# Performance work log

Measured on AMD Instinct MI355X. Metric: run time of the kernel, lower is better.

The kernel has to match this reference:

```python
import jax, jax.numpy as jnp
import numpy as np

N_SRC, N_DST, E, D, OUT = 100000, 20000, 600000, 128, 128

def setup_inputs() -> dict:
    key = jax.random.key(0)
    k1, k2, k3, k4, k5 = jax.random.split(key, 5)
    h = jax.random.normal(k1, (N_SRC, D), dtype=jnp.float32)
    edge_src = jax.random.randint(k2, (E,), 0, N_SRC, dtype=jnp.int64)
    edge_dst = jax.random.randint(k3, (E,), 0, N_DST, dtype=jnp.int64)
    W = jax.random.normal(k4, (OUT, 2 * D), dtype=jnp.float32) * (1.0 / np.sqrt(2 * D))
    b = jax.random.normal(k5, (OUT,), dtype=jnp.float32) * 0.01
    return {"h": h, "edge_src": edge_src, "edge_dst": edge_dst, "W": W, "b": b, "n_dst": N_DST}

def reference(h, edge_src, edge_dst, W, b, n_dst):
    # dst nodes are the first n_dst src nodes (DGL block convention)
    h_dst = h[:n_dst]                                   # [n_dst, D]
    msgs = h[edge_src]                                  # gather: [E, D]
    agg = jax.ops.segment_sum(msgs, edge_dst, num_segments=n_dst)   # [n_dst, D]
    deg = jax.ops.segment_sum(jnp.ones(edge_src.shape, h.dtype), edge_dst, num_segments=n_dst)
    h_neigh = agg / jnp.maximum(deg, 1.0)[:, None]      # mean; 0-degree -> 0
    z = jnp.concatenate([h_dst, h_neigh], axis=1)       # [n_dst, 2D]
    return jax.nn.relu(z @ W.T + b)                     # [n_dst, OUT]
```

## Files before the change

kernel.cpp:

```cpp
#include <hip/hip_runtime.h>

#define DFEAT 128
#define KDIM  256
#define CAP   128
#define WSTR  264

typedef __attribute__((ext_vector_type(8))) short bf16x8;
typedef __attribute__((ext_vector_type(4))) float f32x4;

__device__ __forceinline__ float bflo(unsigned int u) {
    union { unsigned int i; float f; } v; v.i = u << 16; return v.f;
}
__device__ __forceinline__ float bfhi(unsigned int u) {
    union { unsigned int i; float f; } v; v.i = u & 0xffff0000u; return v.f;
}
__device__ __forceinline__ unsigned short f2bf(float f) {
    union { float f; unsigned int i; } v; v.f = f;
    unsigned int r = (v.i + 0x7fffu + ((v.i >> 16) & 1u)) >> 16;
    return (unsigned short)r;
}
__device__ __forceinline__ unsigned int pack2(float x, float y) {
    return ((unsigned int)f2bf(y) << 16) | (unsigned int)f2bf(x);
}
__device__ __forceinline__ uint4 cvt8(const float* p) {
    float4 a = *(const float4*)p;
    float4 b = *(const float4*)(p + 4);
    return make_uint4(pack2(a.x, a.y), pack2(a.z, a.w),
                      pack2(b.x, b.y), pack2(b.z, b.w));
}

__global__ __launch_bounds__(256) void prep_kernel(
    const float* __restrict__ h, const float* __restrict__ W,
    const int* __restrict__ esrc, const int* __restrict__ edst,
    unsigned short* __restrict__ hbf,
    unsigned short* __restrict__ z,
    unsigned short* __restrict__ Wbf,
    int* __restrict__ cnt, int* __restrict__ sorted,
    int E, int n_chunks, int B_C, int B_H)
{
    int blk = blockIdx.x;
    int tid = threadIdx.x;
    if (blk < B_C) {
        int e0 = blk * 1024 + tid;
        int d[4], s[4];
        bool ok[4];
        #pragma unroll
        for (int r = 0; r < 4; ++r) {
            int e = e0 + r * 256;
            ok[r] = (e < E);
            d[r] = ok[r] ? edst[e] : 0;
            s[r] = ok[r] ? esrc[e] : 0;
        }
        int pos[4];
        #pragma unroll
        for (int r = 0; r < 4; ++r)
            pos[r] = ok[r] ? atomicAdd(&cnt[d[r]], 1) : CAP;
        #pragma unroll
        for (int r = 0; r < 4; ++r)
            if (ok[r] && pos[r] < CAP)
                sorted[(size_t)d[r] * CAP + pos[r]] = s[r];
    } else if (blk < B_C + B_H) {
        int c0 = (blk - B_C) * 1024 + tid;
        #pragma unroll
        for (int r = 0; r < 4; ++r) {
            int t = c0 + r * 256;
            if (t < n_chunks) {
                uint4 v = cvt8(h + (size_t)t * 8);
                if (hbf) {
                    *(uint4*)(hbf + (size_t)t * 8) = v;
                } else {
                    int row = t >> 4;
                    int col = (t & 15) * 8;
                    *(uint4*)(z + (size_t)row * KDIM + col) = v;
                }
            }
        }
    } else {
        int t = (blk - B_C - B_H) * 256 + tid;
        *(uint4*)(Wbf + (size_t)t * 8) = cvt8(W + (size_t)t * 8);
    }
}

__global__ __launch_bounds__(256) void agg_bf16_kernel(
    const unsigned short* __restrict__ hbf, const int* __restrict__ cnt,
    const int* __restrict__ sorted, unsigned short* __restrict__ zn, int n_dst)
{
    int d = blockIdx.x * 4 + (threadIdx.x >> 6);
    if (d >= n_dst) return;
    int lane = threadIdx.x & 63;
    int c = cnt[d]; if (c > CAP) c = CAP;
    const int* seg = sorted + (size_t)d * CAP;
    float ax = 0.f, ay = 0.f;
    const unsigned int* hp = (const unsigned int*)hbf + lane;
    int i = 0;
    for (; i + 7 < c; i += 8) {
        int ix[8];
        #pragma unroll
        for (int r = 0; r < 8; ++r) ix[r] = seg[i + r];
        unsigned int u[8];
        #pragma unroll
        for (int r = 0; r < 8; ++r) u[r] = hp[(size_t)ix[r] * 64];
        #pragma unroll
        for (int r = 0; r < 8; ++r) { ax += bflo(u[r]); ay += bfhi(u[r]); }
    }
    for (; i + 3 < c; i += 4) {
        int i0 = seg[i],     i1 = seg[i + 1];
        int i2 = seg[i + 2], i3 = seg[i + 3];
        unsigned int u0 = hp[(size_t)i0 * 64], u1 = hp[(size_t)i1 * 64];
        unsigned int u2 = hp[(size_t)i2 * 64], u3 = hp[(size_t)i3 * 64];
        ax += bflo(u0) + bflo(u1) + bflo(u2) + bflo(u3);
        ay += bfhi(u0) + bfhi(u1) + bfhi(u2) + bfhi(u3);
    }
    for (; i < c; ++i) {
        unsigned int u = hp[(size_t)seg[i] * 64];
        ax += bflo(u); ay += bfhi(u);
    }
    float inv = 1.0f / fmaxf((float)c, 1.0f);
    ((unsigned int*)zn)[(size_t)d * 64 + lane] = pack2(ax * inv, ay * inv);
}

__global__ __launch_bounds__(256) void agg_f32_kernel(
    const float* __restrict__ h, const int* __restrict__ cnt,
    const int* __restrict__ sorted, unsigned short* __restrict__ z, int n_dst)
{
    int d = blockIdx.x * 4 + (threadIdx.x >> 6);
    if (d >= n_dst) return;
    int lane = threadIdx.x & 63;
    int c = cnt[d]; if (c > CAP) c = CAP;
    const int* seg = sorted + (size_t)d * CAP;
    float ax = 0.f, ay = 0.f;
    const float2* hp = (const float2*)h + lane;
    int i = 0;
    for (; i + 1 < c; i += 2) {
        int i0 = seg[i], i1 = seg[i + 1];
        float2 v0 = hp[(size_t)i0 * 64], v1 = hp[(size_t)i1 * 64];
        ax += v0.x + v1.x; ay += v0.y + v1.y;
    }
    for (; i < c; ++i) {
        float2 v = hp[(size_t)seg[i] * 64];
        ax += v.x; ay += v.y;
    }
    float inv = 1.0f / fmaxf((float)c, 1.0f);
    ((unsigned int*)z)[(size_t)d * 128 + 64 + lane] = pack2(ax * inv, ay * inv);
}

__global__ __launch_bounds__(256) void gemm_kernel(
    const unsigned short* __restrict__ alo, int slo,
    const unsigned short* __restrict__ ahi, int shi,
    const unsigned short* __restrict__ Wbf,
    const float* __restrict__ bias,
    float* __restrict__ out,
    int n_dst)
{
    __shared__ unsigned short Wl[DFEAT][WSTR];

    int tid  = threadIdx.x;
    int wave = tid >> 6;
    int lane = tid & 63;
    int quad = lane >> 4;
    int l16  = lane & 15;
    int m0   = blockIdx.x * 64 + wave * 16;

    #pragma unroll
    for (int i = 0; i < 16; ++i) {
        int u  = i * 256 + tid;
        int n  = u >> 5;
        int kq = (u & 31) * 8;
        *(uint4*)&Wl[n][kq] = *(const uint4*)(Wbf + (size_t)n * KDIM + kq);
    }

    int m_a = m0 + l16;
    if (m_a > n_dst - 1) m_a = n_dst - 1;

    f32x4 acc[8];
    #pragma unroll
    for (int ct = 0; ct < 8; ++ct) acc[ct] = (f32x4){0.f, 0.f, 0.f, 0.f};

    const unsigned short* plo = alo + (size_t)m_a * slo + quad * 8;
    const unsigned short* phi = ahi + (size_t)m_a * shi + quad * 8;

    __syncthreads();

    #pragma unroll
    for (int ks = 0; ks < 8; ++ks) {
        bf16x8 a = (ks < 4) ? *(const bf16x8*)(plo + ks * 32)
                            : *(const bf16x8*)(phi + (ks - 4) * 32);
        #pragma unroll
        for (int ct = 0; ct < 8; ++ct) {
            bf16x8 bb = *(const bf16x8*)&Wl[ct * 16 + l16][ks * 32 + quad * 8];
            acc[ct] = __builtin_amdgcn_mfma_f32_16x16x32_bf16(a, bb, acc[ct], 0, 0, 0);
        }
    }

    #pragma unroll
    for (int ct = 0; ct < 8; ++ct) {
        int n = ct * 16 + l16;
        float bc = bias[n];
        #pragma unroll
        for (int r = 0; r < 4; ++r) {
            int m = m0 + quad * 4 + r;
            if (m < n_dst)
                out[(size_t)m * DFEAT + n] = fmaxf(acc[ct][r] + bc, 0.0f);
        }
    }
}


extern "C" void kernel_launch(void* const* d_in, const int* in_sizes, int n_in,
                              void* d_out, int out_size, void* d_ws, size_t ws_size,
                              hipStream_t stream) {
    const float* h  = (const float*)d_in[0];
    const int* esrc = (const int*)d_in[1];
    const int* edst = (const int*)d_in[2];
    const float* W  = (const float*)d_in[3];
    const float* b  = (const float*)d_in[4];
    float* out      = (float*)d_out;

    const int E     = in_sizes[1];
    const int n_src = in_sizes[0] / DFEAT;
    const int n_dst = out_size / DFEAT;

    size_t hbf_bytes  = (size_t)n_src * DFEAT * 2;
    size_t zn_bytes   = (size_t)n_dst * DFEAT * 2;
    size_t wbf_bytes  = (size_t)DFEAT * KDIM * 2;
    size_t cnt_bytes  = (size_t)n_dst * sizeof(int);
    size_t srt_bytes  = (size_t)n_dst * CAP * sizeof(int);
    bool fast = ws_size >= hbf_bytes + zn_bytes + wbf_bytes + cnt_bytes + srt_bytes;

    char* p = (char*)d_ws;
    unsigned short *hbf, *zn, *Wbf;
    int *cnt, *sorted;
    if (fast) {
        hbf = (unsigned short*)p;            p += hbf_bytes;
        zn  = (unsigned short*)p;            p += zn_bytes;
        Wbf = (unsigned short*)p;            p += wbf_bytes;
        cnt = (int*)p;                       p += cnt_bytes;
        sorted = (int*)p;
    } else {
        hbf = nullptr; zn = nullptr;
        Wbf = (unsigned short*)p;            p += wbf_bytes;
        cnt = (int*)p;                       p += cnt_bytes;
        sorted = (int*)p;
    }

    unsigned short* z = (unsigned short*)d_out;

    (void)hipMemsetAsync(cnt, 0, cnt_bytes, stream);

    int n_chunks = (fast ? n_src : n_dst) * (DFEAT / 8);
    int B_C = (E + 1023) / 1024;
    int B_H = (n_chunks + 1023) / 1024;
    int B_W = (DFEAT * KDIM / 8) / 256;
    prep_kernel<<<B_C + B_H + B_W, 256, 0, stream>>>(
        h, W, esrc, edst, hbf, fast ? nullptr : z, Wbf, cnt, sorted,
        E, n_chunks, B_C, B_H);

    if (fast) {
        agg_bf16_kernel<<<(n_dst + 3) / 4, 256, 0, stream>>>(
            hbf, cnt, sorted, zn, n_dst);
        gemm_kernel<<<(n_dst + 63) / 64, 256, 0, stream>>>(
            hbf, DFEAT, zn, DFEAT, Wbf, b, out, n_dst);
    } else {
        agg_f32_kernel<<<(n_dst + 3) / 4, 256, 0, stream>>>(
            h, cnt, sorted, z, n_dst);
        gemm_kernel<<<(n_dst + 63) / 64, 256, 0, stream>>>(
            z, KDIM, z + DFEAT, KDIM, Wbf, b, out, n_dst);
    }
}
```

Before: 185.1 us.

## Fuse neighbor mean aggregation into GEMM via shared-memory tile

Merges the bf16 aggregation kernel and the GEMM kernel into one kernel. Each block aggregates 32 destination rows into LDS and then runs the MFMA GEMM on them directly, so the zn intermediate is never written to or read back from global memory and one launch is removed. In exchange, each block reloads the full 64KB W tile for only 32 rows, which doubles W staging traffic. Occupancy drops because of the larger LDS footprint, and each wave gathers 8 rows serially, which may reduce latency hiding for the gather.

New measurement: 208.1 us. 12.4% more time.

```diff
diff --git a/kernel.cpp b/kernel.cpp
--- a/kernel.cpp
+++ b/kernel.cpp
@@ -4,6 +4,8 @@
 #define KDIM  256
 #define CAP   128
 #define WSTR  264
+#define ZSTRU 68
+#define RTILE 32
 
 typedef __attribute__((ext_vector_type(8))) short bf16x8;
 typedef __attribute__((ext_vector_type(4))) float f32x4;
@@ -81,42 +83,105 @@
     }
 }
 
-__global__ __launch_bounds__(256) void agg_bf16_kernel(
-    const unsigned short* __restrict__ hbf, const int* __restrict__ cnt,
-    const int* __restrict__ sorted, unsigned short* __restrict__ zn, int n_dst)
+__global__ __launch_bounds__(256) void fused_kernel(
+    const unsigned short* __restrict__ hbf,
+    const int* __restrict__ cnt,
+    const int* __restrict__ sorted,
+    const unsigned short* __restrict__ Wbf,
+    const float* __restrict__ bias,
+    float* __restrict__ out,
+    int n_dst)
 {
-    int d = blockIdx.x * 4 + (threadIdx.x >> 6);
-    if (d >= n_dst) return;
-    int lane = threadIdx.x & 63;
-    int c = cnt[d]; if (c > CAP) c = CAP;
-    const int* seg = sorted + (size_t)d * CAP;
-    float ax = 0.f, ay = 0.f;
+    __shared__ unsigned short Wl[DFEAT][WSTR];
+    __shared__ unsigned int   znl[RTILE][ZSTRU];
+
+    const int tid  = threadIdx.x;
+    const int wave = tid >> 6;
+    const int lane = tid & 63;
+    const int quad = lane >> 4;
+    const int l16  = lane & 15;
+    const int m0   = blockIdx.x * RTILE;
+
+    #pragma unroll
+    for (int i = 0; i < 16; ++i) {
+        int u  = i * 256 + tid;
+        int n  = u >> 5;
+        int kq = (u & 31) * 8;
+        *(uint4*)&Wl[n][kq] = *(const uint4*)(Wbf + (size_t)n * KDIM + kq);
+    }
+
     const unsigned int* hp = (const unsigned int*)hbf + lane;
-    int i = 0;
-    for (; i + 7 < c; i += 8) {
-        int ix[8];
-        #pragma unroll
-        for (int r = 0; r < 8; ++r) ix[r] = seg[i + r];
-        unsigned int u[8];
-        #pragma unroll
-        for (int r = 0; r < 8; ++r) u[r] = hp[(size_t)ix[r] * 64];
-        #pragma unroll
-        for (int r = 0; r < 8; ++r) { ax += bflo(u[r]); ay += bfhi(u[r]); }
-    }
-    for (; i + 3 < c; i += 4) {
-        int i0 = seg[i],     i1 = seg[i + 1];
-        int i2 = seg[i + 2], i3 = seg[i + 3];
-        unsigned int u0 = hp[(size_t)i0 * 64], u1 = hp[(size_t)i1 * 64];
-        unsigned int u2 = hp[(size_t)i2 * 64], u3 = hp[(size_t)i3 * 64];
-        ax += bflo(u0) + bflo(u1) + bflo(u2) + bflo(u3);
-        ay += bfhi(u0) + bfhi(u1) + bfhi(u2) + bfhi(u3);
-    }
-    for (; i < c; ++i) {
-        unsigned int u = hp[(size_t)seg[i] * 64];
-        ax += bflo(u); ay += bfhi(u);
-    }
-    float inv = 1.0f / fmaxf((float)c, 1.0f);
-    ((unsigned int*)zn)[(size_t)d * 64 + lane] = pack2(ax * inv, ay * inv);
+    for (int t = 0; t < 8; ++t) {
+        int lr = wave * 8 + t;
+        int d  = m0 + lr;
+        if (d >= n_dst) break;
+        int c = cnt[d]; if (c > CAP) c = CAP;
+        const int* seg = sorted + (size_t)d * CAP;
+        float ax = 0.f, ay = 0.f;
+        int i = 0;
+        for (; i + 7 < c; i += 8) {
+            int ix[8];
+            #pragma unroll
+            for (int r = 0; r < 8; ++r) ix[r] = seg[i + r];
+            unsigned int u[8];
+            #pragma unroll
+            for (int r = 0; r < 8; ++r) u[r] = hp[(size_t)ix[r] * 64];
+            #pragma unroll
+            for (int r = 0; r < 8; ++r) { ax += bflo(u[r]); ay += bfhi(u[r]); }
+        }
+        for (; i + 3 < c; i += 4) {
+            int i0 = seg[i],     i1 = seg[i + 1];
+            int i2 = seg[i + 2], i3 = seg[i + 3];
+            unsigned int u0 = hp[(size_t)i0 * 64], u1 = hp[(size_t)i1 * 64];
+            unsigned int u2 = hp[(size_t)i2 * 64], u3 = hp[(size_t)i3 * 64];
+            ax += bflo(u0) + bflo(u1) + bflo(u2) + bflo(u3);
+            ay += bfhi(u0) + bfhi(u1) + bfhi(u2) + bfhi(u3);
+        }
+        for (; i < c; ++i) {
+            unsigned int u = hp[(size_t)seg[i] * 64];
+            ax += bflo(u); ay += bfhi(u);
+        }
+        float inv = 1.0f / fmaxf((float)c, 1.0f);
+        znl[lr][lane] = pack2(ax * inv, ay * inv);
+    }
+    __syncthreads();
+
+    const int r0 = (wave >> 1) * 16;
+    const int c0 = (wave & 1) * 64;
+    int m_a = m0 + r0 + l16;
+    if (m_a > n_dst - 1) m_a = n_dst - 1;
+
+    f32x4 acc[4];
+    #pragma unroll
+    for (int ct = 0; ct < 4; ++ct) acc[ct] = (f32x4){0.f, 0.f, 0.f, 0.f};
+
+    const unsigned short* plo = hbf + (size_t)m_a * DFEAT + quad * 8;
+    #pragma unroll
+    for (int ks = 0; ks < 8; ++ks) {
+        bf16x8 a;
+        if (ks < 4) {
+            a = *(const bf16x8*)(plo + ks * 32);
+        } else {
+            a = *(const bf16x8*)&znl[r0 + l16][(ks - 4) * 16 + quad * 4];
+        }
+        #pragma unroll
+        for (int ct = 0; ct < 4; ++ct) {
+            bf16x8 bb = *(const bf16x8*)&Wl[c0 + ct * 16 + l16][ks * 32 + quad * 8];
+            acc[ct] = __builtin_amdgcn_mfma_f32_16x16x32_bf16(a, bb, acc[ct], 0, 0, 0);
+        }
+    }
+
+    #pragma unroll
+    for (int ct = 0; ct < 4; ++ct) {
+        int n = c0 + ct * 16 + l16;
+        float bc = bias[n];
+        #pragma unroll
+        for (int r = 0; r < 4; ++r) {
+            int m = m0 + r0 + quad * 4 + r;
+            if (m < n_dst)
+                out[(size_t)m * DFEAT + n] = fmaxf(acc[ct][r] + bc, 0.0f);
+        }
+    }
 }
 
 __global__ __launch_bounds__(256) void agg_f32_kernel(
@@ -153,7 +218,6 @@
     int n_dst)
 {
     __shared__ unsigned short Wl[DFEAT][WSTR];
-
     int tid  = threadIdx.x;
     int wave = tid >> 6;
     int lane = tid & 63;
@@ -168,19 +232,14 @@
         int kq = (u & 31) * 8;
         *(uint4*)&Wl[n][kq] = *(const uint4*)(Wbf + (size_t)n * KDIM + kq);
     }
-
     int m_a = m0 + l16;
     if (m_a > n_dst - 1) m_a = n_dst - 1;
-
     f32x4 acc[8];
     #pragma unroll
     for (int ct = 0; ct < 8; ++ct) acc[ct] = (f32x4){0.f, 0.f, 0.f, 0.f};
-
     const unsigned short* plo = alo + (size_t)m_a * slo + quad * 8;
     const unsigned short* phi = ahi + (size_t)m_a * shi + quad * 8;
-
     __syncthreads();
-
     #pragma unroll
     for (int ks = 0; ks < 8; ++ks) {
         bf16x8 a = (ks < 4) ? *(const bf16x8*)(plo + ks * 32)
@@ -191,7 +250,6 @@
             acc[ct] = __builtin_amdgcn_mfma_f32_16x16x32_bf16(a, bb, acc[ct], 0, 0, 0);
         }
     }
-
     #pragma unroll
     for (int ct = 0; ct < 8; ++ct) {
         int n = ct * 16 + l16;
@@ -221,23 +279,21 @@
     const int n_dst = out_size / DFEAT;
 
     size_t hbf_bytes  = (size_t)n_src * DFEAT * 2;
-    size_t zn_bytes   = (size_t)n_dst * DFEAT * 2;
     size_t wbf_bytes  = (size_t)DFEAT * KDIM * 2;
     size_t cnt_bytes  = (size_t)n_dst * sizeof(int);
     size_t srt_bytes  = (size_t)n_dst * CAP * sizeof(int);
-    bool fast = ws_size >= hbf_bytes + zn_bytes + wbf_bytes + cnt_bytes + srt_bytes;
+    bool fast = ws_size >= hbf_bytes + wbf_bytes + cnt_bytes + srt_bytes;
 
     char* p = (char*)d_ws;
-    unsigned short *hbf, *zn, *Wbf;
+    unsigned short *hbf, *Wbf;
     int *cnt, *sorted;
     if (fast) {
         hbf = (unsigned short*)p;            p += hbf_bytes;
-        zn  = (unsigned short*)p;            p += zn_bytes;
         Wbf = (unsigned short*)p;            p += wbf_bytes;
         cnt = (int*)p;                       p += cnt_bytes;
         sorted = (int*)p;
     } else {
-        hbf = nullptr; zn = nullptr;
+        hbf = nullptr;
         Wbf = (unsigned short*)p;            p += wbf_bytes;
         cnt = (int*)p;                       p += cnt_bytes;
         sorted = (int*)p;
@@ -256,10 +312,8 @@
         E, n_chunks, B_C, B_H);
 
     if (fast) {
-        agg_bf16_kernel<<<(n_dst + 3) / 4, 256, 0, stream>>>(
-            hbf, cnt, sorted, zn, n_dst);
-        gemm_kernel<<<(n_dst + 63) / 64, 256, 0, stream>>>(
-            hbf, DFEAT, zn, DFEAT, Wbf, b, out, n_dst);
+        fused_kernel<<<(n_dst + RTILE - 1) / RTILE, 256, 0, stream>>>(
+            hbf, cnt, sorted, Wbf, b, out, n_dst);
     } else {
         agg_f32_kernel<<<(n_dst + 3) / 4, 256, 0, stream>>>(
             h, cnt, sorted, z, n_dst);
```
